# Kernel tuning notes

Hardware: AMD Instinct MI355X
Metric: run time of the kernel (lower is better)

The kernel has to match this reference:

```python
import jax, jax.numpy as jnp
import numpy as np

B, L, H, W, C = 2, 32, 16, 16, 32  # L must equal channels for the view() to be consistent
CH = L  # conv channel count


def setup_inputs() -> dict:
    key = jax.random.key(0)
    k1, k2, k3, k4, k5 = jax.random.split(key, 5)
    return {
        "inputs": jax.random.normal(k1, (B, L, H, W, C), dtype=jnp.float32),
        "W1": jax.random.normal(k2, (CH // 2, CH), dtype=jnp.float32) * 0.1,
        "b1": jax.random.normal(k3, (CH // 2,), dtype=jnp.float32) * 0.1,
        "W2": jax.random.normal(k4, (CH, CH), dtype=jnp.float32) * 0.1,
        "b2": jax.random.normal(k5, (CH,), dtype=jnp.float32) * 0.1,
        "gamma": jnp.ones((1,), dtype=jnp.float32),
    }


def reference(inputs, W1, b1, W2, b2, gamma):
    b, l, h, w, c = inputs.shape
    n = l * h * w  # flattened 'spatial' positions after the (buggy-but-faithful) reshape
    # conv1x1 over dim-1 (torch Conv3d treats dim-1 as channels)
    x1 = jnp.einsum('ol,blhwc->bohwc', W1, inputs) + b1[None, :, None, None, None]
    # permute (0,4,1,2,3) then view(b, c//2, l*h*w)
    x1 = jnp.transpose(x1, (0, 4, 1, 2, 3)).reshape(b, c // 2, n)
    # attn[b, i, j] = sum_k x1[b, k, i] * x1[b, k, j]; softmax over last dim
    attn = jax.nn.softmax(jnp.einsum('bki,bkj->bij', x1, x1), axis=-1)  # [b, n, n]
    x2 = jnp.einsum('ol,blhwc->bohwc', W2, inputs) + b2[None, :, None, None, None]
    x2 = jnp.transpose(x2, (0, 4, 1, 2, 3)).reshape(b, c, n)
    # x2 @ attn^T : out[b, c, i] = sum_j x2[b, c, j] * attn[b, i, j]
    out = jnp.einsum('bcj,bij->bci', x2, attn)
    out = jnp.transpose(out.reshape(b, c, l, h, w), (0, 2, 3, 4, 1))
    return out * gamma + inputs
```

## Files before the change

### kernel.cpp

```cpp
#include <hip/hip_runtime.h>
#include <hip/hip_bf16.h>
#include <math.h>

typedef __bf16 bf16x8 __attribute__((ext_vector_type(8)));
typedef __bf16 bf16x2 __attribute__((ext_vector_type(2)));
typedef short  s16x2  __attribute__((ext_vector_type(2)));
typedef short  s16x4  __attribute__((ext_vector_type(4)));
typedef float  floatx16 __attribute__((ext_vector_type(16)));

#define KQ_ELEMS (2 * 8192 * 16)
#define OPART_OFF 1572864
#define SQRT_LOG2E 1.2011224087864498f
#define LSPLIT 3

__global__ __launch_bounds__(512) void proj_kernel(
    const float* __restrict__ in, const float* __restrict__ W1,
    const float* __restrict__ b1, const float* __restrict__ W2,
    const float* __restrict__ b2,
    __hip_bfloat16* __restrict__ Kq, __hip_bfloat16* __restrict__ Vswz)
{
    __shared__ float Xs[32][32];
    __shared__ float W1s[16 * 32];
    __shared__ float W2s[32 * 32];
    const int t = threadIdx.x;
    const int bid = blockIdx.x;
    const int b = bid >> 8;
    const int hw = bid & 255;

    {
        int l = t >> 4, cs = (t & 15) * 2;
        float2 v = *(const float2*)(in + (((size_t)b * 32 + l) * 256 + hw) * 32 + cs);
        *(float2*)&Xs[l][cs] = v;
    }
    if (t < 128) *(float4*)&W1s[t * 4] = *(const float4*)(W1 + t * 4);
    if (t < 256) *(float4*)&W2s[t * 4] = *(const float4*)(W2 + t * 4);
    __syncthreads();

    const int c = t & 31;
    const int g = t >> 5;

    {
        int o = g;
        float a0 = b1[o], a1 = 0.f;
#pragma unroll
        for (int l = 0; l < 16; ++l) {
            a0 += W1s[o * 32 + l] * Xs[l][c];
            a1 += W1s[o * 32 + 16 + l] * Xs[16 + l][c];
        }
        float acc = a0 + a1;
        int k = c >> 1;
        int i = (c & 1) * 4096 + o * 256 + hw;
        Kq[((size_t)b * 8192 + i) * 16 + k] = __float2bfloat16(acc * SQRT_LOG2E);
    }
#pragma unroll
    for (int oo = 0; oo < 2; ++oo) {
        int o = g * 2 + oo;
        float a0 = b2[o], a1 = 0.f;
#pragma unroll
        for (int l = 0; l < 16; ++l) {
            a0 += W2s[o * 32 + l] * Xs[l][c];
            a1 += W2s[o * 32 + 16 + l] * Xs[16 + l][c];
        }
        float acc = a0 + a1;
        int j = o * 256 + hw;
        int jt = j >> 5, rem = j & 31;
        int gg = rem >> 3, hh = (rem >> 2) & 1, idx = rem & 3;
        Vswz[(size_t)b * 262144 + jt * 1024 + gg * 256 + hh * 128 + c * 4 + idx] =
            __float2bfloat16(acc);
    }
}

__global__ __launch_bounds__(256, 4) void flash_kernel(
    const __hip_bfloat16* __restrict__ Kq, const __hip_bfloat16* __restrict__ Vswz,
    __hip_bfloat16* __restrict__ Opart, float* __restrict__ Lpart)
{
    const int t = threadIdx.x;
    const int lane = t & 63;
    const int wv = t >> 6;
    const int m = lane & 31;
    const int h = lane >> 5;

    const int bid = blockIdx.x;
    const int s = bid & ((1 << LSPLIT) - 1);
    const int itile = (bid >> LSPLIT) & 63;
    const int b = bid >> (LSPLIT + 6);
    const int i0 = itile * 128 + wv * 32;
    const int niter = (8192 >> LSPLIT) >> 5;
    const int jt0 = s * niter;

    const __hip_bfloat16* Kb = Kq + (size_t)b * 8192 * 16;
    const __hip_bfloat16* Vb = Vswz + (size_t)b * 262144 + h * 128 + m * 4;

    const bf16x8 bq = *(const bf16x8*)(Kb + (size_t)(i0 + m) * 16 + h * 8);

    floatx16 oa = {}, ob = {};
    float2 l01 = {0.f, 0.f}, l23 = {0.f, 0.f};

#pragma unroll 2
    for (int it = 0; it < niter; ++it) {
        const int jt = jt0 + it;
        bf16x8 ak = *(const bf16x8*)(Kb + (size_t)(jt * 32 + m) * 16 + h * 8);
        s16x4 vf0 = *(const s16x4*)(Vb + (size_t)jt * 1024 + 0);
        s16x4 vf1 = *(const s16x4*)(Vb + (size_t)jt * 1024 + 256);
        s16x4 vf2 = *(const s16x4*)(Vb + (size_t)jt * 1024 + 512);
        s16x4 vf3 = *(const s16x4*)(Vb + (size_t)jt * 1024 + 768);

        floatx16 sc = __builtin_amdgcn_mfma_f32_32x32x16_bf16(ak, bq, (floatx16){}, 0, 0, 0);

#pragma unroll
        for (int g = 0; g < 4; ++g) {
            float e0 = __builtin_amdgcn_exp2f(sc[4 * g + 0]);
            float e1 = __builtin_amdgcn_exp2f(sc[4 * g + 1]);
            float e2 = __builtin_amdgcn_exp2f(sc[4 * g + 2]);
            float e3 = __builtin_amdgcn_exp2f(sc[4 * g + 3]);
            l01.x += e0; l01.y += e1; l23.x += e2; l23.y += e3;
#if defined(__has_builtin) && __has_builtin(__builtin_amdgcn_cvt_pk_bf16_f32)
            bf16x2 plo = __builtin_amdgcn_cvt_pk_bf16_f32(e0, e1);
            bf16x2 phi = __builtin_amdgcn_cvt_pk_bf16_f32(e2, e3);
#else
            bf16x2 plo = {(__bf16)e0, (__bf16)e1};
            bf16x2 phi = {(__bf16)e2, (__bf16)e3};
#endif
            s16x2 lo = __builtin_bit_cast(s16x2, plo);
            s16x2 hi = __builtin_bit_cast(s16x2, phi);
            s16x4 pb = {lo[0], lo[1], hi[0], hi[1]};
            s16x4 vf = (g == 0) ? vf0 : (g == 1) ? vf1 : (g == 2) ? vf2 : vf3;
            if (g < 2)
                oa = __builtin_amdgcn_mfma_f32_32x32x8bf16_1k(pb, vf, oa, 0, 0, 0);
            else
                ob = __builtin_amdgcn_mfma_f32_32x32x8bf16_1k(pb, vf, ob, 0, 0, 0);
        }
    }

    oa = oa + ob;
    float l = (l01.x + l01.y) + (l23.x + l23.y);
    l += __shfl_xor(l, 32);
    const float rinv = __builtin_amdgcn_rcpf(l);

#pragma unroll
    for (int r = 0; r < 16; ++r) {
        int iloc = (r & 3) + 8 * (r >> 2) + 4 * h;
        float lr = __shfl(rinv, iloc);
        size_t row = (size_t)b * 8192 + i0 + iloc;
        Opart[((row << LSPLIT) | s) * 32 + m] = __float2bfloat16(oa[r] * lr);
    }
    if (h == 0)
        Lpart[(((size_t)b * 8192 + i0 + m) << LSPLIT) | s] = l;
}

__global__ __launch_bounds__(256) void combine_kernel(
    const unsigned short* __restrict__ Opart, const float* __restrict__ Lpart,
    const float* __restrict__ in, const float* __restrict__ gamma,
    float* __restrict__ out)
{
    const int gid = blockIdx.x * 256 + threadIdx.x;
    const int row = gid >> 4;
    const int c2 = (gid & 15) * 2;
    const unsigned short* op = Opart + (((size_t)row << LSPLIT)) * 32 + c2;
    const float* lp = Lpart + ((size_t)row << LSPLIT);
    float ax = 0.f, ay = 0.f;
    float lsum = 0.f;
#pragma unroll
    for (int s = 0; s < (1 << LSPLIT); ++s) {
        ushort2 u = *(const ushort2*)(op + s * 32);
        float ls = lp[s];
        ax += ls * __uint_as_float((unsigned)u.x << 16);
        ay += ls * __uint_as_float((unsigned)u.y << 16);
        lsum += ls;
    }
    const size_t base = (size_t)row * 32 + c2;
    float2 x = *(const float2*)(in + base);
    const float gl = gamma[0] / lsum;
    float2 r;
    r.x = ax * gl + x.x;
    r.y = ay * gl + x.y;
    *(float2*)(out + base) = r;
}

extern "C" void kernel_launch(void* const* d_in, const int* in_sizes, int n_in,
                              void* d_out, int out_size, void* d_ws, size_t ws_size,
                              hipStream_t stream) {
    const float* in = (const float*)d_in[0];
    const float* W1 = (const float*)d_in[1];
    const float* b1 = (const float*)d_in[2];
    const float* W2 = (const float*)d_in[3];
    const float* b2 = (const float*)d_in[4];
    const float* gamma = (const float*)d_in[5];
    float* out = (float*)d_out;

    __hip_bfloat16* Kq = (__hip_bfloat16*)d_ws;
    __hip_bfloat16* Vswz = Kq + KQ_ELEMS;
    __hip_bfloat16* Opart = (__hip_bfloat16*)((char*)d_ws + OPART_OFF);
    float* Lpart = (float*)(Opart + ((size_t)16384 << LSPLIT) * 32);

    proj_kernel<<<512, 512, 0, stream>>>(in, W1, b1, W2, b2, Kq, Vswz);
    flash_kernel<<<2 * 64 * (1 << LSPLIT), 256, 0, stream>>>(Kq, Vswz, Opart, Lpart);
    combine_kernel<<<1024, 256, 0, stream>>>((const unsigned short*)Opart, Lpart, in, gamma, out);
}
```

Baseline: 101.7 us.

## Prefetch next K/V tile in registers, raise split count, vectorize combine loads

The flash kernel now loads the next tile's K and V fragments into registers before running the MFMA and exp work on the current tile. This software-pipelines global load latency behind compute. The key-dimension split goes from 8 to 16 partitions, which gives more blocks and a shorter loop per block, and the min-occupancy hint is removed from launch_bounds so the compiler has more registers for the double-buffered values. The combine kernel now reads the per-split normalizers as float4. The cost is doubled partial-output traffic written to and read back from the workspace, and possibly lower occupancy.

Result: slower. 110.4 us (+8.6%).

```diff
diff --git a/kernel.cpp b/kernel.cpp
--- a/kernel.cpp
+++ b/kernel.cpp
@@ -11,7 +11,7 @@
 #define KQ_ELEMS (2 * 8192 * 16)
 #define OPART_OFF 1572864
 #define SQRT_LOG2E 1.2011224087864498f
-#define LSPLIT 3
+#define LSPLIT 4
 
 __global__ __launch_bounds__(512) void proj_kernel(
     const float* __restrict__ in, const float* __restrict__ W1,
@@ -70,7 +70,7 @@
     }
 }
 
-__global__ __launch_bounds__(256, 4) void flash_kernel(
+__global__ __launch_bounds__(256) void flash_kernel(
     const __hip_bfloat16* __restrict__ Kq, const __hip_bfloat16* __restrict__ Vswz,
     __hip_bfloat16* __restrict__ Opart, float* __restrict__ Lpart)
 {
@@ -96,16 +96,26 @@
     floatx16 oa = {}, ob = {};
     float2 l01 = {0.f, 0.f}, l23 = {0.f, 0.f};
 
+    bf16x8 ak = *(const bf16x8*)(Kb + (size_t)(jt0 * 32 + m) * 16 + h * 8);
+    s16x4 vf0 = *(const s16x4*)(Vb + (size_t)jt0 * 1024 + 0);
+    s16x4 vf1 = *(const s16x4*)(Vb + (size_t)jt0 * 1024 + 256);
+    s16x4 vf2 = *(const s16x4*)(Vb + (size_t)jt0 * 1024 + 512);
+    s16x4 vf3 = *(const s16x4*)(Vb + (size_t)jt0 * 1024 + 768);
+
 #pragma unroll 2
     for (int it = 0; it < niter; ++it) {
-        const int jt = jt0 + it;
-        bf16x8 ak = *(const bf16x8*)(Kb + (size_t)(jt * 32 + m) * 16 + h * 8);
-        s16x4 vf0 = *(const s16x4*)(Vb + (size_t)jt * 1024 + 0);
-        s16x4 vf1 = *(const s16x4*)(Vb + (size_t)jt * 1024 + 256);
-        s16x4 vf2 = *(const s16x4*)(Vb + (size_t)jt * 1024 + 512);
-        s16x4 vf3 = *(const s16x4*)(Vb + (size_t)jt * 1024 + 768);
-
-        floatx16 sc = __builtin_amdgcn_mfma_f32_32x32x16_bf16(ak, bq, (floatx16){}, 0, 0, 0);
+        const bf16x8 cak = ak;
+        const s16x4 cv0 = vf0, cv1 = vf1, cv2 = vf2, cv3 = vf3;
+        if (it + 1 < niter) {
+            const int jn = jt0 + it + 1;
+            ak  = *(const bf16x8*)(Kb + (size_t)(jn * 32 + m) * 16 + h * 8);
+            vf0 = *(const s16x4*)(Vb + (size_t)jn * 1024 + 0);
+            vf1 = *(const s16x4*)(Vb + (size_t)jn * 1024 + 256);
+            vf2 = *(const s16x4*)(Vb + (size_t)jn * 1024 + 512);
+            vf3 = *(const s16x4*)(Vb + (size_t)jn * 1024 + 768);
+        }
+
+        floatx16 sc = __builtin_amdgcn_mfma_f32_32x32x16_bf16(cak, bq, (floatx16){}, 0, 0, 0);
 
 #pragma unroll
         for (int g = 0; g < 4; ++g) {
@@ -124,7 +134,7 @@
             s16x2 lo = __builtin_bit_cast(s16x2, plo);
             s16x2 hi = __builtin_bit_cast(s16x2, phi);
             s16x4 pb = {lo[0], lo[1], hi[0], hi[1]};
-            s16x4 vf = (g == 0) ? vf0 : (g == 1) ? vf1 : (g == 2) ? vf2 : vf3;
+            s16x4 vf = (g == 0) ? cv0 : (g == 1) ? cv1 : (g == 2) ? cv2 : cv3;
             if (g < 2)
                 oa = __builtin_amdgcn_mfma_f32_32x32x8bf16_1k(pb, vf, oa, 0, 0, 0);
             else
@@ -158,15 +168,22 @@
     const int c2 = (gid & 15) * 2;
     const unsigned short* op = Opart + (((size_t)row << LSPLIT)) * 32 + c2;
     const float* lp = Lpart + ((size_t)row << LSPLIT);
+    float ls[1 << LSPLIT];
+#pragma unroll
+    for (int q = 0; q < (1 << LSPLIT) / 4; ++q) {
+        float4 lv = *(const float4*)(lp + q * 4);
+        ls[q * 4 + 0] = lv.x; ls[q * 4 + 1] = lv.y;
+        ls[q * 4 + 2] = lv.z; ls[q * 4 + 3] = lv.w;
+    }
     float ax = 0.f, ay = 0.f;
     float lsum = 0.f;
 #pragma unroll
     for (int s = 0; s < (1 << LSPLIT); ++s) {
         ushort2 u = *(const ushort2*)(op + s * 32);
-        float ls = lp[s];
-        ax += ls * __uint_as_float((unsigned)u.x << 16);
-        ay += ls * __uint_as_float((unsigned)u.y << 16);
-        lsum += ls;
+        float l = ls[s];
+        ax += l * __uint_as_float((unsigned)u.x << 16);
+        ay += l * __uint_as_float((unsigned)u.y << 16);
+        lsum += l;
     }
     const size_t base = (size_t)row * 32 + c2;
     float2 x = *(const float2*)(in + base);
```

## Use 32x32x16 MFMA for PV with lane-shuffled P and prefetched K/V

Applied to the files above, without the earlier changes.

Reorders the V swizzle layout so each lane holds 8 bf16 values, and replaces the four 32x32x8 PV MFMAs per tile with two 32x32x16 MFMAs. The P fragments are assembled across lane halves with xor-32 shuffles. K and V loads for the next tile are software-prefetched into registers, and the occupancy hint on the flash kernel is dropped. The combine kernel now reads the split-L partial sums as two float4 loads. The aim is fewer MFMA issues and hidden load latency, paid for with extra shuffles and selects and higher register pressure.

After: 107.4 us. 5.6% more time.

```diff
diff --git a/kernel.cpp b/kernel.cpp
--- a/kernel.cpp
+++ b/kernel.cpp
@@ -7,6 +7,7 @@
 typedef short  s16x2  __attribute__((ext_vector_type(2)));
 typedef short  s16x4  __attribute__((ext_vector_type(4)));
 typedef float  floatx16 __attribute__((ext_vector_type(16)));
+typedef unsigned u32x4 __attribute__((ext_vector_type(4)));
 
 #define KQ_ELEMS (2 * 8192 * 16)
 #define OPART_OFF 1572864
@@ -62,15 +63,14 @@
             a1 += W2s[o * 32 + 16 + l] * Xs[16 + l][c];
         }
         float acc = a0 + a1;
-        int j = o * 256 + hw;
-        int jt = j >> 5, rem = j & 31;
-        int gg = rem >> 3, hh = (rem >> 2) & 1, idx = rem & 3;
-        Vswz[(size_t)b * 262144 + jt * 1024 + gg * 256 + hh * 128 + c * 4 + idx] =
+        int jt = o * 8 + (hw >> 5);
+        int gp = (hw >> 4) & 1, hh = (hw >> 3) & 1, idx = hw & 7;
+        Vswz[(size_t)b * 262144 + jt * 1024 + gp * 512 + hh * 256 + c * 8 + idx] =
             __float2bfloat16(acc);
     }
 }
 
-__global__ __launch_bounds__(256, 4) void flash_kernel(
+__global__ __launch_bounds__(256) void flash_kernel(
     const __hip_bfloat16* __restrict__ Kq, const __hip_bfloat16* __restrict__ Vswz,
     __hip_bfloat16* __restrict__ Opart, float* __restrict__ Lpart)
 {
@@ -79,6 +79,7 @@
     const int wv = t >> 6;
     const int m = lane & 31;
     const int h = lane >> 5;
+    const bool hi = (h != 0);
 
     const int bid = blockIdx.x;
     const int s = bid & ((1 << LSPLIT) - 1);
@@ -89,47 +90,66 @@
     const int jt0 = s * niter;
 
     const __hip_bfloat16* Kb = Kq + (size_t)b * 8192 * 16;
-    const __hip_bfloat16* Vb = Vswz + (size_t)b * 262144 + h * 128 + m * 4;
+    const __hip_bfloat16* Vb = Vswz + (size_t)b * 262144 + h * 256 + m * 8;
 
     const bf16x8 bq = *(const bf16x8*)(Kb + (size_t)(i0 + m) * 16 + h * 8);
 
     floatx16 oa = {}, ob = {};
     float2 l01 = {0.f, 0.f}, l23 = {0.f, 0.f};
 
+    bf16x8 ak = *(const bf16x8*)(Kb + (size_t)(jt0 * 32 + m) * 16 + h * 8);
+    bf16x8 vb0 = *(const bf16x8*)(Vb + (size_t)jt0 * 1024 + 0);
+    bf16x8 vb1 = *(const bf16x8*)(Vb + (size_t)jt0 * 1024 + 512);
+
 #pragma unroll 2
     for (int it = 0; it < niter; ++it) {
-        const int jt = jt0 + it;
-        bf16x8 ak = *(const bf16x8*)(Kb + (size_t)(jt * 32 + m) * 16 + h * 8);
-        s16x4 vf0 = *(const s16x4*)(Vb + (size_t)jt * 1024 + 0);
-        s16x4 vf1 = *(const s16x4*)(Vb + (size_t)jt * 1024 + 256);
-        s16x4 vf2 = *(const s16x4*)(Vb + (size_t)jt * 1024 + 512);
-        s16x4 vf3 = *(const s16x4*)(Vb + (size_t)jt * 1024 + 768);
-
-        floatx16 sc = __builtin_amdgcn_mfma_f32_32x32x16_bf16(ak, bq, (floatx16){}, 0, 0, 0);
-
+        const bf16x8 cak = ak;
+        const bf16x8 cv0 = vb0, cv1 = vb1;
+        if (it + 1 < niter) {
+            const int jn = jt0 + it + 1;
+            ak  = *(const bf16x8*)(Kb + (size_t)(jn * 32 + m) * 16 + h * 8);
+            vb0 = *(const bf16x8*)(Vb + (size_t)jn * 1024 + 0);
+            vb1 = *(const bf16x8*)(Vb + (size_t)jn * 1024 + 512);
+        }
+
+        floatx16 sc = __builtin_amdgcn_mfma_f32_32x32x16_bf16(cak, bq, (floatx16){}, 0, 0, 0);
+
+        float e[16];
+#pragma unroll
+        for (int r = 0; r < 16; ++r) e[r] = __builtin_amdgcn_exp2f(sc[r]);
 #pragma unroll
         for (int g = 0; g < 4; ++g) {
-            float e0 = __builtin_amdgcn_exp2f(sc[4 * g + 0]);
-            float e1 = __builtin_amdgcn_exp2f(sc[4 * g + 1]);
-            float e2 = __builtin_amdgcn_exp2f(sc[4 * g + 2]);
-            float e3 = __builtin_amdgcn_exp2f(sc[4 * g + 3]);
-            l01.x += e0; l01.y += e1; l23.x += e2; l23.y += e3;
+            l01.x += e[4 * g + 0]; l01.y += e[4 * g + 1];
+            l23.x += e[4 * g + 2]; l23.y += e[4 * g + 3];
+        }
+
+        unsigned cp[4][2];
+#pragma unroll
+        for (int g = 0; g < 4; ++g) {
+#pragma unroll
+            for (int p = 0; p < 2; ++p) {
 #if defined(__has_builtin) && __has_builtin(__builtin_amdgcn_cvt_pk_bf16_f32)
-            bf16x2 plo = __builtin_amdgcn_cvt_pk_bf16_f32(e0, e1);
-            bf16x2 phi = __builtin_amdgcn_cvt_pk_bf16_f32(e2, e3);
+                bf16x2 pk = __builtin_amdgcn_cvt_pk_bf16_f32(e[4 * g + 2 * p], e[4 * g + 2 * p + 1]);
 #else
-            bf16x2 plo = {(__bf16)e0, (__bf16)e1};
-            bf16x2 phi = {(__bf16)e2, (__bf16)e3};
+                bf16x2 pk = {(__bf16)e[4 * g + 2 * p], (__bf16)e[4 * g + 2 * p + 1]};
 #endif
-            s16x2 lo = __builtin_bit_cast(s16x2, plo);
-            s16x2 hi = __builtin_bit_cast(s16x2, phi);
-            s16x4 pb = {lo[0], lo[1], hi[0], hi[1]};
-            s16x4 vf = (g == 0) ? vf0 : (g == 1) ? vf1 : (g == 2) ? vf2 : vf3;
-            if (g < 2)
-                oa = __builtin_amdgcn_mfma_f32_32x32x8bf16_1k(pb, vf, oa, 0, 0, 0);
-            else
-                ob = __builtin_amdgcn_mfma_f32_32x32x8bf16_1k(pb, vf, ob, 0, 0, 0);
-        }
+                cp[g][p] = __builtin_bit_cast(unsigned, pk);
+            }
+        }
+
+        unsigned x00 = __shfl_xor((int)cp[0][0], 32), x01 = __shfl_xor((int)cp[0][1], 32);
+        unsigned x10 = __shfl_xor((int)cp[1][0], 32), x11 = __shfl_xor((int)cp[1][1], 32);
+        unsigned x20 = __shfl_xor((int)cp[2][0], 32), x21 = __shfl_xor((int)cp[2][1], 32);
+        unsigned x30 = __shfl_xor((int)cp[3][0], 32), x31 = __shfl_xor((int)cp[3][1], 32);
+        u32x4 pa0u = { hi ? x10 : cp[0][0], hi ? x11 : cp[0][1],
+                       hi ? cp[1][0] : x00, hi ? cp[1][1] : x01 };
+        u32x4 pa1u = { hi ? x30 : cp[2][0], hi ? x31 : cp[2][1],
+                       hi ? cp[3][0] : x20, hi ? cp[3][1] : x21 };
+        bf16x8 pa0 = __builtin_bit_cast(bf16x8, pa0u);
+        bf16x8 pa1 = __builtin_bit_cast(bf16x8, pa1u);
+
+        oa = __builtin_amdgcn_mfma_f32_32x32x16_bf16(pa0, cv0, oa, 0, 0, 0);
+        ob = __builtin_amdgcn_mfma_f32_32x32x16_bf16(pa1, cv1, ob, 0, 0, 0);
     }
 
     oa = oa + ob;
@@ -158,12 +178,15 @@
     const int c2 = (gid & 15) * 2;
     const unsigned short* op = Opart + (((size_t)row << LSPLIT)) * 32 + c2;
     const float* lp = Lpart + ((size_t)row << LSPLIT);
+    float4 l0 = *(const float4*)(lp);
+    float4 l1 = *(const float4*)(lp + 4);
+    float ls8[8] = {l0.x, l0.y, l0.z, l0.w, l1.x, l1.y, l1.z, l1.w};
     float ax = 0.f, ay = 0.f;
     float lsum = 0.f;
 #pragma unroll
     for (int s = 0; s < (1 << LSPLIT); ++s) {
         ushort2 u = *(const ushort2*)(op + s * 32);
-        float ls = lp[s];
+        float ls = ls8[s];
         ax += ls * __uint_as_float((unsigned)u.x << 16);
         ay += ls * __uint_as_float((unsigned)u.y << 16);
         lsum += ls;
```
